# Kernel tuning notes

Measured on AMD Instinct MI355X. Metric: run time of the kernel, lower is better.

Reference implementation:

```python
import jax, jax.numpy as jnp
import numpy as np

N_NEURONS, D_MODEL, D_FF, N_PATTERNS, K_PATTERNS = 2048, 1024, 4096, 64, 4
B, S, K = 4, 2048, 8


def setup_inputs() -> dict:
    key = jax.random.key(0)
    ks = jax.random.split(key, 10)
    return {
        "x": jax.random.normal(ks[0], (B, S, D_MODEL), jnp.float32),
        "router_out": jax.random.normal(ks[1], (B, S, D_MODEL), jnp.float32),
        "topk_neuron_idx": jax.random.randint(ks[2], (B, S, K), 0, N_NEURONS),
        "topk_neuron_weights": jax.random.uniform(ks[3], (B, S, K), jnp.float32),
        "selected_neurons": jax.random.normal(ks[4], (B, S, K, D_MODEL), jnp.float32),
        "pattern_queries": jax.random.normal(ks[5], (N_PATTERNS, D_MODEL), jnp.float32) * 0.02,
        "gates": jax.random.normal(ks[6], (N_PATTERNS, D_FF), jnp.float32) * 0.02,
        "up_w": jax.random.normal(ks[7], (D_FF, D_MODEL), jnp.float32) / np.sqrt(D_MODEL),
        "up_b": jnp.zeros((D_FF,), jnp.float32),
        "down_w": jax.random.normal(ks[8], (D_MODEL, D_FF), jnp.float32) / np.sqrt(D_FF),
        "down_b": jnp.zeros((D_MODEL,), jnp.float32),
    }


def reference(x, router_out, topk_neuron_idx, topk_neuron_weights, selected_neurons,
              pattern_queries, gates, up_w, up_b, down_w, down_b):
    D = selected_neurons.shape[-1]
    # pattern scoring: [P, B, S, K]
    sim = jnp.einsum('pd,bskd->pbsk', pattern_queries, selected_neurons) / jnp.sqrt(jnp.float32(D))
    pattern_scores = jnp.einsum('pbsk,bsk->bsp', sim, topk_neuron_weights)  # weighted sum over K, permuted
    topk_scores, topk_pattern_idx = jax.lax.top_k(pattern_scores, K_PATTERNS)  # [B,S,k]
    topk_pattern_weights = jax.nn.softmax(topk_scores, axis=-1)
    selected_gates = gates[topk_pattern_idx]  # [B,S,k,d_ff]
    ffn_gate = jnp.einsum('bsk,bskf->bsf', topk_pattern_weights, selected_gates)
    h = jnp.einsum('bsd,fd->bsf', x, up_w) + up_b
    h = jax.nn.gelu(h * jax.nn.sigmoid(ffn_gate), approximate=False)
    return jnp.einsum('bsf,df->bsd', h, down_w) + down_b
```

## Files before the change

### kernel.cpp

```cpp
#include <hip/hip_runtime.h>
#include <hip/hip_bf16.h>
#include <math.h>

#define R_   8192
#define DM   1024
#define DFF  4096
#define NP   64
#define KN   8

typedef __bf16 bf16x8 __attribute__((ext_vector_type(8)));
typedef float  f32x4  __attribute__((ext_vector_type(4)));

__device__ __forceinline__ unsigned short f2bf(float f) {
  union { float f; unsigned u; } v; v.f = f;
  unsigned u = v.u;
  return (unsigned short)((u + 0x7FFFu + ((u >> 16) & 1u)) >> 16);
}

__device__ __forceinline__ float dot4(const float4 a, const float4 b) {
  return a.x * b.x + a.y * b.y + a.z * b.z + a.w * b.w;
}

__device__ __forceinline__ void fma4(float4& a, float w, const float4 s) {
  a.x += w * s.x; a.y += w * s.y; a.z += w * s.z; a.w += w * s.w;
}

__global__ __launch_bounds__(256) void cvt_bf16_kernel(
    const float* __restrict__ in, unsigned short* __restrict__ out, int n8) {
  int i = blockIdx.x * 256 + threadIdx.x;
  if (i >= n8) return;
  const float4* p = (const float4*)in + (size_t)i * 2;
  float4 a = p[0], b = p[1];
  uint4 r;
  r.x = (unsigned)f2bf(a.x) | ((unsigned)f2bf(a.y) << 16);
  r.y = (unsigned)f2bf(a.z) | ((unsigned)f2bf(a.w) << 16);
  r.z = (unsigned)f2bf(b.x) | ((unsigned)f2bf(b.y) << 16);
  r.w = (unsigned)f2bf(b.z) | ((unsigned)f2bf(b.w) << 16);
  ((uint4*)out)[i] = r;
}

__global__ __launch_bounds__(256) void vcomp_kernel(
    const float* __restrict__ sn,
    const float* __restrict__ tw,
    float* __restrict__ v)
{
  const int r = blockIdx.x;
  const int t = threadIdx.x;
  float w[KN];
#pragma unroll
  for (int k = 0; k < KN; ++k) w[k] = tw[(size_t)r * KN + k];
  const float* base = sn + (size_t)r * (KN * DM) + t * 4;
  float4 a = {0.f, 0.f, 0.f, 0.f};
#pragma unroll
  for (int k = 0; k < KN; ++k) fma4(a, w[k], *(const float4*)(base + k * DM));
  *(float4*)(v + (size_t)r * DM + t * 4) = a;
}

__global__ __launch_bounds__(256, 2) void score_kernel(
    const float* __restrict__ v,
    const float* __restrict__ pq,
    int*   __restrict__ out_idx,
    float* __restrict__ out_w)
{
  const int lane = threadIdx.x & 63;
  const int wave = threadIdx.x >> 6;
  const int pos0 = (blockIdx.x * 4 + wave) * 4;

  float4 vr[4][4];
#pragma unroll
  for (int p = 0; p < 4; ++p) {
    const float4* s = (const float4*)(v + (size_t)(pos0 + p) * DM + lane * 16);
    vr[p][0] = s[0]; vr[p][1] = s[1]; vr[p][2] = s[2]; vr[p][3] = s[3];
  }

  float sreg[4];
#pragma unroll 1
  for (int pat = 0; pat < NP; ++pat) {
    const float4* q = (const float4*)(pq + pat * DM + lane * 16);
    const float4 q0 = q[0], q1 = q[1], q2 = q[2], q3 = q[3];
    float part[4];
#pragma unroll
    for (int p = 0; p < 4; ++p)
      part[p] = dot4(q0, vr[p][0]) + dot4(q1, vr[p][1]) +
                dot4(q2, vr[p][2]) + dot4(q3, vr[p][3]);
#pragma unroll
    for (int off = 32; off >= 1; off >>= 1) {
#pragma unroll
      for (int p = 0; p < 4; ++p)
        part[p] += __shfl_xor(part[p], off, 64);
    }
    if (lane == pat) {
#pragma unroll
      for (int p = 0; p < 4; ++p) sreg[p] = part[p] * 0.03125f;
    }
  }

#pragma unroll
  for (int p = 0; p < 4; ++p) {
    float cur = sreg[p];
    float m0, m1, m2, m3; int i0, i1, i2, i3;
#define ARGMAX_STEP(MV, MI)                                   \
    {                                                         \
      float bv = cur; int bi = lane;                          \
      _Pragma("unroll")                                       \
      for (int off = 32; off >= 1; off >>= 1) {               \
        float ov = __shfl_xor(bv, off, 64);                   \
        int   oi = __shfl_xor(bi, off, 64);                   \
        if (ov > bv || (ov == bv && oi < bi)) { bv = ov; bi = oi; } \
      }                                                       \
      MV = bv; MI = bi;                                       \
      if (lane == bi) cur = -3.0e38f;                         \
    }
    ARGMAX_STEP(m0, i0) ARGMAX_STEP(m1, i1) ARGMAX_STEP(m2, i2) ARGMAX_STEP(m3, i3)
#undef ARGMAX_STEP
    const float e1 = __expf(m1 - m0), e2 = __expf(m2 - m0), e3 = __expf(m3 - m0);
    const float inv = 1.f / (1.f + e1 + e2 + e3);
    if (lane < 4) {
      const int r = pos0 + p;
      const int myi = (lane == 0) ? i0 : (lane == 1) ? i1 : (lane == 2) ? i2 : i3;
      const float mye = (lane == 0) ? 1.f : (lane == 1) ? e1 : (lane == 2) ? e2 : e3;
      out_idx[r * 4 + lane] = myi;
      out_w[r * 4 + lane] = mye * inv;
    }
  }
}

__device__ __forceinline__ void gll16(const void* g, void* l) {
  __builtin_amdgcn_global_load_lds(
      (const __attribute__((address_space(1))) unsigned int*)g,
      (__attribute__((address_space(3))) unsigned int*)l, 16, 0, 0);
}

template <int K, int N, int MODE>
__global__ __launch_bounds__(256, 2) void gemm_kernel(
    const unsigned short* __restrict__ A,
    const unsigned short* __restrict__ Bm,
    const float* __restrict__ bias,
    const int*   __restrict__ pidx,
    const float* __restrict__ pwt,
    const float* __restrict__ gates,
    void* __restrict__ Cout)
{
  __shared__ __align__(16) unsigned short As[128 * 32];
  __shared__ __align__(16) unsigned short Bs[128 * 32];
  const int tid  = threadIdx.x;
  const int lane = tid & 63;
  const int wid  = tid >> 6;
  const int wr   = wid >> 1;
  const int wc   = wid & 1;
  constexpr int NB = N / 128;
  const int brow = blockIdx.x / NB;
  const int bcol = blockIdx.x % NB;

  const unsigned short* Ab = A  + (size_t)brow * 128 * K;
  const unsigned short* Bb = Bm + (size_t)bcol * 128 * K;

  f32x4 acc[4][4];
#pragma unroll
  for (int m = 0; m < 4; ++m)
#pragma unroll
    for (int n = 0; n < 4; ++n)
      acc[m][n] = (f32x4){0.f, 0.f, 0.f, 0.f};

  const int srow = tid >> 2;
  const int scol = (tid & 3) * 8;
  char* ldsA = (char*)As + (tid >> 6) * 1024;
  char* ldsB = (char*)Bs + (tid >> 6) * 1024;

  const int arow = wr * 64 + (lane & 15);
  const int bro  = wc * 64 + (lane & 15);
  const int koff = (lane >> 4) * 8;

  for (int k0 = 0; k0 < K; k0 += 32) {
    if (k0) __syncthreads();
    gll16(Ab + (size_t)srow * K + k0 + scol,        ldsA);
    gll16(Ab + (size_t)(srow + 64) * K + k0 + scol, ldsA + 4096);
    gll16(Bb + (size_t)srow * K + k0 + scol,        ldsB);
    gll16(Bb + (size_t)(srow + 64) * K + k0 + scol, ldsB + 4096);
    __syncthreads();

    bf16x8 af[4], bfr[4];
#pragma unroll
    for (int m = 0; m < 4; ++m)
      af[m] = *(const bf16x8*)(As + (arow + m * 16) * 32 + koff);
#pragma unroll
    for (int n = 0; n < 4; ++n)
      bfr[n] = *(const bf16x8*)(Bs + (bro + n * 16) * 32 + koff);
#pragma unroll
    for (int m = 0; m < 4; ++m)
#pragma unroll
      for (int n = 0; n < 4; ++n)
        acc[m][n] = __builtin_amdgcn_mfma_f32_16x16x32_bf16(
            af[m], bfr[n], acc[m][n], 0, 0, 0);
  }

  const int crow0 = brow * 128 + wr * 64;
  const int ccol0 = bcol * 128 + wc * 64 + (lane & 15);
  const int rsub  = (lane >> 4) * 4;

  if (MODE == 0) {
    unsigned short* H = (unsigned short*)Cout;
#pragma unroll
    for (int m = 0; m < 4; ++m) {
      const int rbase = crow0 + m * 16 + rsub;
      int   ia[4][4];
      float wa[4][4];
#pragma unroll
      for (int j = 0; j < 4; ++j) {
        const int4   iq = *(const int4*)(pidx + (size_t)(rbase + j) * 4);
        const float4 wq = *(const float4*)(pwt + (size_t)(rbase + j) * 4);
        ia[j][0] = iq.x; ia[j][1] = iq.y; ia[j][2] = iq.z; ia[j][3] = iq.w;
        wa[j][0] = wq.x; wa[j][1] = wq.y; wa[j][2] = wq.z; wa[j][3] = wq.w;
      }
#pragma unroll
      for (int n = 0; n < 4; ++n) {
        const int col = ccol0 + n * 16;
        const float ub = bias[col];
#pragma unroll
        for (int j = 0; j < 4; ++j) {
          float g = wa[j][0] * gates[(size_t)ia[j][0] * DFF + col]
                  + wa[j][1] * gates[(size_t)ia[j][1] * DFF + col]
                  + wa[j][2] * gates[(size_t)ia[j][2] * DFF + col]
                  + wa[j][3] * gates[(size_t)ia[j][3] * DFF + col];
          const float u   = acc[m][n][j] + ub;
          const float val = u * (1.f / (1.f + __expf(-g)));
          const float h   = 0.5f * val * (1.f + erff(val * 0.70710678118654752f));
          H[(size_t)(rbase + j) * N + col] = f2bf(h);
        }
      }
    }
  } else {
    float* O = (float*)Cout;
#pragma unroll
    for (int m = 0; m < 4; ++m) {
      const int rbase = crow0 + m * 16 + rsub;
#pragma unroll
      for (int n = 0; n < 4; ++n) {
        const int col = ccol0 + n * 16;
        const float db = bias[col];
#pragma unroll
        for (int j = 0; j < 4; ++j)
          O[(size_t)(rbase + j) * N + col] = acc[m][n][j] + db;
      }
    }
  }
}

extern "C" void kernel_launch(void* const* d_in, const int* in_sizes, int n_in,
                              void* d_out, int out_size, void* d_ws, size_t ws_size,
                              hipStream_t stream) {
  const float* x     = (const float*)d_in[0];
  const float* tw    = (const float*)d_in[3];
  const float* sn    = (const float*)d_in[4];
  const float* pq    = (const float*)d_in[5];
  const float* gates = (const float*)d_in[6];
  const float* upw   = (const float*)d_in[7];
  const float* upb   = (const float*)d_in[8];
  const float* dnw   = (const float*)d_in[9];
  const float* dnb   = (const float*)d_in[10];
  float* out = (float*)d_out;

  char* p = (char*)d_ws;
  unsigned short* xb  = (unsigned short*)p; p += (size_t)R_ * DM * 2;
  unsigned short* uwb = (unsigned short*)p; p += (size_t)DFF * DM * 2;
  unsigned short* dwb = (unsigned short*)p; p += (size_t)DM * DFF * 2;
  unsigned short* H   = (unsigned short*)p; p += (size_t)R_ * DFF * 2;
  int*   pidx = (int*)p;   p += (size_t)R_ * 4 * sizeof(int);
  float* pwt  = (float*)p; p += (size_t)R_ * 4 * sizeof(float);
  float* vbuf = (float*)p; p += (size_t)R_ * DM * sizeof(float);

  cvt_bf16_kernel<<<(R_ * DM / 8) / 256, 256, 0, stream>>>(x, xb, R_ * DM / 8);
  cvt_bf16_kernel<<<(DFF * DM / 8) / 256, 256, 0, stream>>>(upw, uwb, DFF * DM / 8);
  cvt_bf16_kernel<<<(DM * DFF / 8) / 256, 256, 0, stream>>>(dnw, dwb, DM * DFF / 8);

  vcomp_kernel<<<R_, 256, 0, stream>>>(sn, tw, vbuf);
  score_kernel<<<R_ / 16, 256, 0, stream>>>(vbuf, pq, pidx, pwt);

  gemm_kernel<DM, DFF, 0><<<(R_ / 128) * (DFF / 128), 256, 0, stream>>>(
      xb, uwb, upb, pidx, pwt, gates, (void*)H);
  gemm_kernel<DFF, DM, 1><<<(R_ / 128) * (DM / 128), 256, 0, stream>>>(
      H, dwb, dnb, nullptr, nullptr, nullptr, (void*)out);
}
```

Before: 408.5 us.

## Replace LDS-staged GEMMs with direct-to-register double-buffered loads and larger tiles

Both GEMMs now load MFMA fragments straight from global memory into registers with a two-stage software double buffer, instead of staging tiles through LDS with two barriers per K step. Blocks grow to 512 threads with 256x256 (up-projection) and 256x128 (down-projection) tiles, a blockIdx swizzle improves L2 locality, and MFMA loops are bracketed with s_setprio. The aim is to remove LDS round trips and barrier stalls and to overlap loads with matrix math. In exchange, register pressure rises sharply (acc[8][4] plus two fragment sets), and without LDS sharing each wave reads its own operands from global memory, which raises cache traffic.

```diff
diff --git a/kernel.cpp b/kernel.cpp
--- a/kernel.cpp
+++ b/kernel.cpp
@@ -125,123 +125,155 @@
   }
 }
 
-__device__ __forceinline__ void gll16(const void* g, void* l) {
-  __builtin_amdgcn_global_load_lds(
-      (const __attribute__((address_space(1))) unsigned int*)g,
-      (__attribute__((address_space(3))) unsigned int*)l, 16, 0, 0);
-}
-
-template <int K, int N, int MODE>
-__global__ __launch_bounds__(256, 2) void gemm_kernel(
+
+#define MMLOOP(MF, ACCOFF, FA, FB)                                          \
+  __builtin_amdgcn_s_setprio(1);                                            \
+  _Pragma("unroll") for (int m_ = 0; m_ < MF; ++m_)                         \
+  _Pragma("unroll") for (int n_ = 0; n_ < 4; ++n_)                          \
+    acc[(ACCOFF) + m_][n_] = __builtin_amdgcn_mfma_f32_16x16x32_bf16(       \
+        FA[m_], FB[n_], acc[(ACCOFF) + m_][n_], 0, 0, 0);                   \
+  __builtin_amdgcn_s_setprio(0);
+
+__global__ __launch_bounds__(512, 2) void gemm1_kernel(
     const unsigned short* __restrict__ A,
     const unsigned short* __restrict__ Bm,
     const float* __restrict__ bias,
     const int*   __restrict__ pidx,
     const float* __restrict__ pwt,
     const float* __restrict__ gates,
-    void* __restrict__ Cout)
+    unsigned short* __restrict__ H)
 {
-  __shared__ __align__(16) unsigned short As[128 * 32];
-  __shared__ __align__(16) unsigned short Bs[128 * 32];
-  const int tid  = threadIdx.x;
-  const int lane = tid & 63;
-  const int wid  = tid >> 6;
-  const int wr   = wid >> 1;
-  const int wc   = wid & 1;
-  constexpr int NB = N / 128;
-  const int brow = blockIdx.x / NB;
-  const int bcol = blockIdx.x % NB;
-
-  const unsigned short* Ab = A  + (size_t)brow * 128 * K;
-  const unsigned short* Bb = Bm + (size_t)bcol * 128 * K;
+  constexpr int K_ = 1024, NT = 32;
+  const int lane = threadIdx.x & 63, wid = threadIdx.x >> 6;
+  const int wr = wid >> 2, wc = wid & 3;
+  const int cpx = gridDim.x >> 3;
+  const int swzb = ((int)blockIdx.x & 7) * cpx + ((int)blockIdx.x >> 3);
+  const int brow = swzb >> 4, bcol = swzb & 15;
+
+  const unsigned short* Ap =
+      A + (size_t)(brow * 256 + wr * 128 + (lane & 15)) * K_ + (lane >> 4) * 8;
+  const unsigned short* Bp =
+      Bm + (size_t)(bcol * 256 + wc * 64 + (lane & 15)) * K_ + (lane >> 4) * 8;
+
+  f32x4 acc[8][4];
+#pragma unroll
+  for (int m = 0; m < 8; ++m)
+#pragma unroll
+    for (int n = 0; n < 4; ++n) acc[m][n] = (f32x4){0.f, 0.f, 0.f, 0.f};
+
+  bf16x8 fa0[8], fb0[4], fa1[8], fb1[4];
+
+#define LD1(FA, FB, KT)                                                     \
+  { _Pragma("unroll") for (int m_ = 0; m_ < 8; ++m_)                        \
+      FA[m_] = *(const bf16x8*)(Ap + m_ * 16 * K_ + (KT) * 32);             \
+    _Pragma("unroll") for (int n_ = 0; n_ < 4; ++n_)                        \
+      FB[n_] = *(const bf16x8*)(Bp + n_ * 16 * K_ + (KT) * 32); }
+
+  LD1(fa0, fb0, 0)
+#pragma unroll 1
+  for (int kt = 0; kt < NT - 2; kt += 2) {
+    LD1(fa1, fb1, kt + 1)
+    MMLOOP(8, 0, fa0, fb0)
+    LD1(fa0, fb0, kt + 2)
+    MMLOOP(8, 0, fa1, fb1)
+  }
+  LD1(fa1, fb1, NT - 1)
+  MMLOOP(8, 0, fa0, fb0)
+  MMLOOP(8, 0, fa1, fb1)
+#undef LD1
+
+  const int crow0 = brow * 256 + wr * 128;
+  const int ccol0 = bcol * 256 + wc * 64 + (lane & 15);
+  const int rsub  = (lane >> 4) * 4;
+#pragma unroll
+  for (int m = 0; m < 8; ++m) {
+    const int rbase = crow0 + m * 16 + rsub;
+    int   ia[4][4];
+    float wa[4][4];
+#pragma unroll
+    for (int j = 0; j < 4; ++j) {
+      const int4   iq = *(const int4*)(pidx + (size_t)(rbase + j) * 4);
+      const float4 wq = *(const float4*)(pwt + (size_t)(rbase + j) * 4);
+      ia[j][0] = iq.x; ia[j][1] = iq.y; ia[j][2] = iq.z; ia[j][3] = iq.w;
+      wa[j][0] = wq.x; wa[j][1] = wq.y; wa[j][2] = wq.z; wa[j][3] = wq.w;
+    }
+#pragma unroll
+    for (int n = 0; n < 4; ++n) {
+      const int col = ccol0 + n * 16;
+      const float ub = bias[col];
+#pragma unroll
+      for (int j = 0; j < 4; ++j) {
+        float g = wa[j][0] * gates[(size_t)ia[j][0] * DFF + col]
+                + wa[j][1] * gates[(size_t)ia[j][1] * DFF + col]
+                + wa[j][2] * gates[(size_t)ia[j][2] * DFF + col]
+                + wa[j][3] * gates[(size_t)ia[j][3] * DFF + col];
+        const float u   = acc[m][n][j] + ub;
+        const float val = u * (1.f / (1.f + __expf(-g)));
+        const float h   = 0.5f * val * (1.f + erff(val * 0.70710678118654752f));
+        H[(size_t)(rbase + j) * DFF + col] = f2bf(h);
+      }
+    }
+  }
+}
+
+__global__ __launch_bounds__(512, 2) void gemm2_kernel(
+    const unsigned short* __restrict__ A,
+    const unsigned short* __restrict__ Bm,
+    const float* __restrict__ bias,
+    float* __restrict__ O)
+{
+  constexpr int K_ = 4096, NT = 128;
+  const int lane = threadIdx.x & 63, wid = threadIdx.x >> 6;
+  const int wr = wid >> 1, wc = wid & 1;
+  const int cpx = gridDim.x >> 3;
+  const int swzb = ((int)blockIdx.x & 7) * cpx + ((int)blockIdx.x >> 3);
+  const int brow = swzb >> 3, bcol = swzb & 7;
+
+  const unsigned short* Ap =
+      A + (size_t)(brow * 256 + wr * 64 + (lane & 15)) * K_ + (lane >> 4) * 8;
+  const unsigned short* Bp =
+      Bm + (size_t)(bcol * 128 + wc * 64 + (lane & 15)) * K_ + (lane >> 4) * 8;
 
   f32x4 acc[4][4];
 #pragma unroll
   for (int m = 0; m < 4; ++m)
 #pragma unroll
-    for (int n = 0; n < 4; ++n)
-      acc[m][n] = (f32x4){0.f, 0.f, 0.f, 0.f};
-
-  const int srow = tid >> 2;
-  const int scol = (tid & 3) * 8;
-  char* ldsA = (char*)As + (tid >> 6) * 1024;
-  char* ldsB = (char*)Bs + (tid >> 6) * 1024;
-
-  const int arow = wr * 64 + (lane & 15);
-  const int bro  = wc * 64 + (lane & 15);
-  const int koff = (lane >> 4) * 8;
-
-  for (int k0 = 0; k0 < K; k0 += 32) {
-    if (k0) __syncthreads();
-    gll16(Ab + (size_t)srow * K + k0 + scol,        ldsA);
-    gll16(Ab + (size_t)(srow + 64) * K + k0 + scol, ldsA + 4096);
-    gll16(Bb + (size_t)srow * K + k0 + scol,        ldsB);
-    gll16(Bb + (size_t)(srow + 64) * K + k0 + scol, ldsB + 4096);
-    __syncthreads();
-
-    bf16x8 af[4], bfr[4];
-#pragma unroll
-    for (int m = 0; m < 4; ++m)
-      af[m] = *(const bf16x8*)(As + (arow + m * 16) * 32 + koff);
-#pragma unroll
-    for (int n = 0; n < 4; ++n)
-      bfr[n] = *(const bf16x8*)(Bs + (bro + n * 16) * 32 + koff);
-#pragma unroll
-    for (int m = 0; m < 4; ++m)
-#pragma unroll
-      for (int n = 0; n < 4; ++n)
-        acc[m][n] = __builtin_amdgcn_mfma_f32_16x16x32_bf16(
-            af[m], bfr[n], acc[m][n], 0, 0, 0);
-  }
-
-  const int crow0 = brow * 128 + wr * 64;
+    for (int n = 0; n < 4; ++n) acc[m][n] = (f32x4){0.f, 0.f, 0.f, 0.f};
+
+  bf16x8 fa0[4], fb0[4], fa1[4], fb1[4];
+
+#define LD2(FA, FB, KT)                                                     \
+  { _Pragma("unroll") for (int m_ = 0; m_ < 4; ++m_)                        \
+      FA[m_] = *(const bf16x8*)(Ap + m_ * 16 * K_ + (KT) * 32);             \
+    _Pragma("unroll") for (int n_ = 0; n_ < 4; ++n_)                        \
+      FB[n_] = *(const bf16x8*)(Bp + n_ * 16 * K_ + (KT) * 32); }
+
+  LD2(fa0, fb0, 0)
+#pragma unroll 1
+  for (int kt = 0; kt < NT - 2; kt += 2) {
+    LD2(fa1, fb1, kt + 1)
+    MMLOOP(4, 0, fa0, fb0)
+    LD2(fa0, fb0, kt + 2)
+    MMLOOP(4, 0, fa1, fb1)
+  }
+  LD2(fa1, fb1, NT - 1)
+  MMLOOP(4, 0, fa0, fb0)
+  MMLOOP(4, 0, fa1, fb1)
+#undef LD2
+
+  const int crow0 = brow * 256 + wr * 64;
   const int ccol0 = bcol * 128 + wc * 64 + (lane & 15);
   const int rsub  = (lane >> 4) * 4;
-
-  if (MODE == 0) {
-    unsigned short* H = (unsigned short*)Cout;
-#pragma unroll
-    for (int m = 0; m < 4; ++m) {
-      const int rbase = crow0 + m * 16 + rsub;
-      int   ia[4][4];
-      float wa[4][4];
-#pragma unroll
-      for (int j = 0; j < 4; ++j) {
-        const int4   iq = *(const int4*)(pidx + (size_t)(rbase + j) * 4);
-        const float4 wq = *(const float4*)(pwt + (size_t)(rbase + j) * 4);
-        ia[j][0] = iq.x; ia[j][1] = iq.y; ia[j][2] = iq.z; ia[j][3] = iq.w;
-        wa[j][0] = wq.x; wa[j][1] = wq.y; wa[j][2] = wq.z; wa[j][3] = wq.w;
-      }
-#pragma unroll
-      for (int n = 0; n < 4; ++n) {
-        const int col = ccol0 + n * 16;
-        const float ub = bias[col];
-#pragma unroll
-        for (int j = 0; j < 4; ++j) {
-          float g = wa[j][0] * gates[(size_t)ia[j][0] * DFF + col]
-                  + wa[j][1] * gates[(size_t)ia[j][1] * DFF + col]
-                  + wa[j][2] * gates[(size_t)ia[j][2] * DFF + col]
-                  + wa[j][3] * gates[(size_t)ia[j][3] * DFF + col];
-          const float u   = acc[m][n][j] + ub;
-          const float val = u * (1.f / (1.f + __expf(-g)));
-          const float h   = 0.5f * val * (1.f + erff(val * 0.70710678118654752f));
-          H[(size_t)(rbase + j) * N + col] = f2bf(h);
-        }
-      }
-    }
-  } else {
-    float* O = (float*)Cout;
-#pragma unroll
-    for (int m = 0; m < 4; ++m) {
-      const int rbase = crow0 + m * 16 + rsub;
-#pragma unroll
-      for (int n = 0; n < 4; ++n) {
-        const int col = ccol0 + n * 16;
-        const float db = bias[col];
-#pragma unroll
-        for (int j = 0; j < 4; ++j)
-          O[(size_t)(rbase + j) * N + col] = acc[m][n][j] + db;
-      }
+#pragma unroll
+  for (int m = 0; m < 4; ++m) {
+    const int rbase = crow0 + m * 16 + rsub;
+#pragma unroll
+    for (int n = 0; n < 4; ++n) {
+      const int col = ccol0 + n * 16;
+      const float db = bias[col];
+#pragma unroll
+      for (int j = 0; j < 4; ++j)
+        O[(size_t)(rbase + j) * DM + col] = acc[m][n][j] + db;
     }
   }
 }
@@ -276,8 +308,8 @@
   vcomp_kernel<<<R_, 256, 0, stream>>>(sn, tw, vbuf);
   score_kernel<<<R_ / 16, 256, 0, stream>>>(vbuf, pq, pidx, pwt);
 
-  gemm_kernel<DM, DFF, 0><<<(R_ / 128) * (DFF / 128), 256, 0, stream>>>(
-      xb, uwb, upb, pidx, pwt, gates, (void*)H);
-  gemm_kernel<DFF, DM, 1><<<(R_ / 128) * (DM / 128), 256, 0, stream>>>(
-      H, dwb, dnb, nullptr, nullptr, nullptr, (void*)out);
-}
+  gemm1_kernel<<<(R_ / 256) * (DFF / 256), 512, 0, stream>>>(
+      xb, uwb, upb, pidx, pwt, gates, H);
+  gemm2_kernel<<<(R_ / 256) * (DM / 128), 512, 0, stream>>>(
+      H, dwb, dnb, out);
+}
```

Result: slower. 630.6 us (+54.4%).

## Rewrite GEMM with 256x128 tiles, triple-buffered LDS pipeline and swizzled layout

Applied to the files above, without the earlier changes.

Replaces the single-buffered 128x128 BK=32 GEMM with a 512-thread 256x128 tile kernel using BK=64, a three-stage global_load_lds pipeline with explicit vmcnt waits, XOR-swizzled LDS to avoid bank conflicts, and a block-index swizzle for L2 locality. It aims to hide global load latency and raise MFMA utilisation that the old load-sync-compute loop lacked. It uses 144KB of dynamic shared memory, which allows only one block per CU, and depends on hand-placed barriers and waitcnts being correct.

```diff
diff --git a/kernel.cpp b/kernel.cpp
--- a/kernel.cpp
+++ b/kernel.cpp
@@ -131,8 +131,10 @@
       (__attribute__((address_space(3))) unsigned int*)l, 16, 0, 0);
 }
 
-template <int K, int N, int MODE>
-__global__ __launch_bounds__(256, 2) void gemm_kernel(
+#define VMC(N) asm volatile("s_waitcnt vmcnt(%0)" ::"i"(N) : "memory")
+
+template <int K_, int NT, int NBN, int MODE>
+__global__ __launch_bounds__(512) void gemm_kernel(
     const unsigned short* __restrict__ A,
     const unsigned short* __restrict__ Bm,
     const float* __restrict__ bias,
@@ -141,60 +143,87 @@
     const float* __restrict__ gates,
     void* __restrict__ Cout)
 {
-  __shared__ __align__(16) unsigned short As[128 * 32];
-  __shared__ __align__(16) unsigned short Bs[128 * 32];
-  const int tid  = threadIdx.x;
-  const int lane = tid & 63;
-  const int wid  = tid >> 6;
-  const int wr   = wid >> 1;
-  const int wc   = wid & 1;
-  constexpr int NB = N / 128;
-  const int brow = blockIdx.x / NB;
-  const int bcol = blockIdx.x % NB;
-
-  const unsigned short* Ab = A  + (size_t)brow * 128 * K;
-  const unsigned short* Bb = Bm + (size_t)bcol * 128 * K;
+  extern __shared__ char smem[];
+  const int tid = threadIdx.x, lane = tid & 63, wid = tid >> 6;
+  const int wr = wid >> 1, wc = wid & 1;
+
+  const int cpx = gridDim.x >> 3;
+  const int swzb = ((int)blockIdx.x & 7) * cpx + ((int)blockIdx.x >> 3);
+  int brow, bcol;
+  if (MODE == 0) { brow = swzb / NBN; bcol = swzb % NBN; }
+  else           { bcol = swzb >> 5;  brow = swzb & 31;  }
+
+  const unsigned short* Ab = A  + (size_t)brow * 256 * K_;
+  const unsigned short* Bb = Bm + (size_t)bcol * 128 * K_;
+
+  const size_t aoff = (size_t)(wid * 8 + (lane >> 3)) * K_ +
+                      ((lane & 7) ^ (lane >> 3)) * 8;
+  const int sw0 = (((lane >> 4))     ^ (lane & 7)) * 16;
+  const int sw1 = ((4 + (lane >> 4)) ^ (lane & 7)) * 16;
+  const int aRdB = wr * 8192 + (lane & 15) * 128;
+  const int bRdB = 32768 + wc * 8192 + (lane & 15) * 128;
 
   f32x4 acc[4][4];
 #pragma unroll
   for (int m = 0; m < 4; ++m)
 #pragma unroll
-    for (int n = 0; n < 4; ++n)
-      acc[m][n] = (f32x4){0.f, 0.f, 0.f, 0.f};
-
-  const int srow = tid >> 2;
-  const int scol = (tid & 3) * 8;
-  char* ldsA = (char*)As + (tid >> 6) * 1024;
-  char* ldsB = (char*)Bs + (tid >> 6) * 1024;
-
-  const int arow = wr * 64 + (lane & 15);
-  const int bro  = wc * 64 + (lane & 15);
-  const int koff = (lane >> 4) * 8;
-
-  for (int k0 = 0; k0 < K; k0 += 32) {
-    if (k0) __syncthreads();
-    gll16(Ab + (size_t)srow * K + k0 + scol,        ldsA);
-    gll16(Ab + (size_t)(srow + 64) * K + k0 + scol, ldsA + 4096);
-    gll16(Bb + (size_t)srow * K + k0 + scol,        ldsB);
-    gll16(Bb + (size_t)(srow + 64) * K + k0 + scol, ldsB + 4096);
-    __syncthreads();
-
-    bf16x8 af[4], bfr[4];
-#pragma unroll
-    for (int m = 0; m < 4; ++m)
-      af[m] = *(const bf16x8*)(As + (arow + m * 16) * 32 + koff);
-#pragma unroll
-    for (int n = 0; n < 4; ++n)
-      bfr[n] = *(const bf16x8*)(Bs + (bro + n * 16) * 32 + koff);
-#pragma unroll
-    for (int m = 0; m < 4; ++m)
-#pragma unroll
-      for (int n = 0; n < 4; ++n)
-        acc[m][n] = __builtin_amdgcn_mfma_f32_16x16x32_bf16(
-            af[m], bfr[n], acc[m][n], 0, 0, 0);
-  }
-
-  const int crow0 = brow * 128 + wr * 64;
+    for (int n = 0; n < 4; ++n) acc[m][n] = (f32x4){0.f, 0.f, 0.f, 0.f};
+
+#define STG(OS, KT) {                                                         \
+    _Pragma("unroll") for (int h_ = 0; h_ < 4; ++h_)                          \
+      gll16(Ab + (KT) * 64 + (size_t)h_ * 64 * K_ + aoff,                     \
+            smem + (OS) + h_ * 8192 + wid * 1024);                            \
+    _Pragma("unroll") for (int h_ = 0; h_ < 2; ++h_)                          \
+      gll16(Bb + (KT) * 64 + (size_t)h_ * 64 * K_ + aoff,                     \
+            smem + (OS) + 32768 + h_ * 8192 + wid * 1024); }
+
+#define RDS(OB, SW)                                                           \
+    { const char* pa = smem + (OB) + aRdB;                                    \
+      const char* pb = smem + (OB) + bRdB;                                    \
+      _Pragma("unroll") for (int m_ = 0; m_ < 4; ++m_)                        \
+        a[m_] = *(const bf16x8*)(pa + m_ * 2048 + (SW));                      \
+      _Pragma("unroll") for (int n_ = 0; n_ < 4; ++n_)                        \
+        b[n_] = *(const bf16x8*)(pb + n_ * 2048 + (SW)); }
+
+#define MIDSYNC                                                               \
+    __builtin_amdgcn_s_barrier();                                             \
+    asm volatile("s_waitcnt lgkmcnt(0)" ::: "memory");                        \
+    __builtin_amdgcn_sched_barrier(0);
+
+#define MF16                                                                  \
+    __builtin_amdgcn_s_setprio(1);                                            \
+    _Pragma("unroll") for (int m_ = 0; m_ < 4; ++m_)                          \
+    _Pragma("unroll") for (int n_ = 0; n_ < 4; ++n_)                          \
+      acc[m_][n_] = __builtin_amdgcn_mfma_f32_16x16x32_bf16(                  \
+          a[m_], b[n_], acc[m_][n_], 0, 0, 0);                                \
+    __builtin_amdgcn_s_setprio(0);                                            \
+    __builtin_amdgcn_s_barrier();
+
+  STG(0, 0)
+  STG(49152, 1)
+  VMC(6);
+  __builtin_amdgcn_s_barrier();
+
+  int o0 = 0, o1 = 49152, o2 = 98304;
+#pragma unroll 1
+  for (int t = 0; t < NT; ++t) {
+    bf16x8 a[4], b[4];
+    RDS(o0, sw0)
+    if (t + 2 < NT) STG(o2, t + 2)
+    MIDSYNC
+    MF16
+    RDS(o0, sw1)
+    if (t < NT - 2) { VMC(6); } else { VMC(0); }
+    MIDSYNC
+    MF16
+    const int tmp = o0; o0 = o1; o1 = o2; o2 = tmp;
+  }
+#undef STG
+#undef RDS
+#undef MIDSYNC
+#undef MF16
+
+  const int crow0 = brow * 256 + wr * 64;
   const int ccol0 = bcol * 128 + wc * 64 + (lane & 15);
   const int rsub  = (lane >> 4) * 4;
 
@@ -225,7 +254,7 @@
           const float u   = acc[m][n][j] + ub;
           const float val = u * (1.f / (1.f + __expf(-g)));
           const float h   = 0.5f * val * (1.f + erff(val * 0.70710678118654752f));
-          H[(size_t)(rbase + j) * N + col] = f2bf(h);
+          H[(size_t)(rbase + j) * DFF + col] = f2bf(h);
         }
       }
     }
@@ -240,7 +269,7 @@
         const float db = bias[col];
 #pragma unroll
         for (int j = 0; j < 4; ++j)
-          O[(size_t)(rbase + j) * N + col] = acc[m][n][j] + db;
+          O[(size_t)(rbase + j) * DM + col] = acc[m][n][j] + db;
       }
     }
   }
@@ -276,8 +305,15 @@
   vcomp_kernel<<<R_, 256, 0, stream>>>(sn, tw, vbuf);
   score_kernel<<<R_ / 16, 256, 0, stream>>>(vbuf, pq, pidx, pwt);
 
-  gemm_kernel<DM, DFF, 0><<<(R_ / 128) * (DFF / 128), 256, 0, stream>>>(
+  auto* k1 = gemm_kernel<DM, 16, 32, 0>;
+  auto* k2 = gemm_kernel<DFF, 64, 8, 1>;
+  hipFuncSetAttribute((const void*)k1,
+                      hipFuncAttributeMaxDynamicSharedMemorySize, 147456);
+  hipFuncSetAttribute((const void*)k2,
+                      hipFuncAttributeMaxDynamicSharedMemorySize, 147456);
+
+  k1<<<(R_ / 256) * (DFF / 128), 512, 147456, stream>>>(
       xb, uwb, upb, pidx, pwt, gates, (void*)H);
-  gemm_kernel<DFF, DM, 1><<<(R_ / 128) * (DM / 128), 256, 0, stream>>>(
+  k2<<<(R_ / 256) * (DM / 128), 512, 147456, stream>>>(
       H, dwb, dnb, nullptr, nullptr, nullptr, (void*)out);
 }
```

After: 380.1 us. 1.07x faster.

## Switch GEMMs to 32x32x16 MFMA with swizzled LDS and larger up-proj tiles

Applied to the files above, without the earlier changes.

Splits the templated GEMM into two specialised kernels that use 32x32x16 bf16 MFMA instead of 16x16x32. The up-projection tile grows to 256x128, block indices are remapped to group work across XCDs, and an XOR swizzle is applied to LDS loads and reads to avoid bank conflicts. The goal is fewer LDS reads per MFMA, better operand reuse and better L2 locality. The tradeoffs are more accumulator registers and more LDS in gemm1, which may reduce occupancy, and the gate epilogue still gathers from global memory per element.

```diff
diff --git a/kernel.cpp b/kernel.cpp
--- a/kernel.cpp
+++ b/kernel.cpp
@@ -10,6 +10,7 @@
 
 typedef __bf16 bf16x8 __attribute__((ext_vector_type(8)));
 typedef float  f32x4  __attribute__((ext_vector_type(4)));
+typedef float  f32x16 __attribute__((ext_vector_type(16)));
 
 __device__ __forceinline__ unsigned short f2bf(float f) {
   union { float f; unsigned u; } v; v.f = f;
@@ -131,117 +132,180 @@
       (__attribute__((address_space(3))) unsigned int*)l, 16, 0, 0);
 }
 
-template <int K, int N, int MODE>
-__global__ __launch_bounds__(256, 2) void gemm_kernel(
+
+__global__ __launch_bounds__(256, 2) void gemm1_kernel(
     const unsigned short* __restrict__ A,
     const unsigned short* __restrict__ Bm,
     const float* __restrict__ bias,
     const int*   __restrict__ pidx,
     const float* __restrict__ pwt,
     const float* __restrict__ gates,
-    void* __restrict__ Cout)
+    unsigned short* __restrict__ H)
 {
-  __shared__ __align__(16) unsigned short As[128 * 32];
-  __shared__ __align__(16) unsigned short Bs[128 * 32];
-  const int tid  = threadIdx.x;
-  const int lane = tid & 63;
-  const int wid  = tid >> 6;
-  const int wr   = wid >> 1;
-  const int wc   = wid & 1;
-  constexpr int NB = N / 128;
-  const int brow = blockIdx.x / NB;
-  const int bcol = blockIdx.x % NB;
-
-  const unsigned short* Ab = A  + (size_t)brow * 128 * K;
-  const unsigned short* Bb = Bm + (size_t)bcol * 128 * K;
-
-  f32x4 acc[4][4];
+  constexpr int K_ = 1024;
+  __shared__ __align__(16) char smem[24576];
+  const int tid = threadIdx.x, lane = tid & 63, wid = tid >> 6;
+  const int wr = wid >> 1, wc = wid & 1;
+
+  const int cpx = gridDim.x >> 3;
+  const int swzb = ((int)blockIdx.x & 7) * cpx + ((int)blockIdx.x >> 3);
+  const int brow = swzb & 31, bcol = swzb >> 5;
+
+  const unsigned short* Ab = A  + (size_t)brow * 256 * K_;
+  const unsigned short* Bb = Bm + (size_t)bcol * 128 * K_;
+
+  const int slotg = ((tid & 3) ^ ((tid >> 3) & 3)) * 8;
+  const int srow  = tid >> 2;
+  const int rA    = (lane & 31) * 64;
+  const int swk0  = (((lane >> 5))     ^ ((lane >> 1) & 3)) * 16;
+  const int swk1  = ((2 + (lane >> 5)) ^ ((lane >> 1) & 3)) * 16;
+
+  f32x16 acc[4][2];
 #pragma unroll
   for (int m = 0; m < 4; ++m)
 #pragma unroll
-    for (int n = 0; n < 4; ++n)
-      acc[m][n] = (f32x4){0.f, 0.f, 0.f, 0.f};
-
-  const int srow = tid >> 2;
-  const int scol = (tid & 3) * 8;
-  char* ldsA = (char*)As + (tid >> 6) * 1024;
-  char* ldsB = (char*)Bs + (tid >> 6) * 1024;
-
-  const int arow = wr * 64 + (lane & 15);
-  const int bro  = wc * 64 + (lane & 15);
-  const int koff = (lane >> 4) * 8;
-
-  for (int k0 = 0; k0 < K; k0 += 32) {
+    for (int n = 0; n < 2; ++n)
+#pragma unroll
+      for (int e = 0; e < 16; ++e) acc[m][n][e] = 0.f;
+
+#pragma unroll 1
+  for (int k0 = 0; k0 < K_; k0 += 32) {
     if (k0) __syncthreads();
-    gll16(Ab + (size_t)srow * K + k0 + scol,        ldsA);
-    gll16(Ab + (size_t)(srow + 64) * K + k0 + scol, ldsA + 4096);
-    gll16(Bb + (size_t)srow * K + k0 + scol,        ldsB);
-    gll16(Bb + (size_t)(srow + 64) * K + k0 + scol, ldsB + 4096);
+#pragma unroll
+    for (int c = 0; c < 4; ++c)
+      gll16(Ab + (size_t)(c * 64 + srow) * K_ + k0 + slotg,
+            smem + c * 4096 + wid * 1024);
+#pragma unroll
+    for (int c = 0; c < 2; ++c)
+      gll16(Bb + (size_t)(c * 64 + srow) * K_ + k0 + slotg,
+            smem + 16384 + c * 4096 + wid * 1024);
     __syncthreads();
 
-    bf16x8 af[4], bfr[4];
-#pragma unroll
-    for (int m = 0; m < 4; ++m)
-      af[m] = *(const bf16x8*)(As + (arow + m * 16) * 32 + koff);
-#pragma unroll
-    for (int n = 0; n < 4; ++n)
-      bfr[n] = *(const bf16x8*)(Bs + (bro + n * 16) * 32 + koff);
-#pragma unroll
-    for (int m = 0; m < 4; ++m)
-#pragma unroll
-      for (int n = 0; n < 4; ++n)
-        acc[m][n] = __builtin_amdgcn_mfma_f32_16x16x32_bf16(
-            af[m], bfr[n], acc[m][n], 0, 0, 0);
+#pragma unroll
+    for (int ks = 0; ks < 2; ++ks) {
+      const int sw = ks ? swk1 : swk0;
+      const char* pa = smem + wr * 8192 + rA + sw;
+      const char* pb = smem + 16384 + wc * 4096 + rA + sw;
+      bf16x8 af[4], bf[2];
+#pragma unroll
+      for (int m = 0; m < 4; ++m) af[m] = *(const bf16x8*)(pa + m * 2048);
+#pragma unroll
+      for (int n = 0; n < 2; ++n) bf[n] = *(const bf16x8*)(pb + n * 2048);
+#pragma unroll
+      for (int m = 0; m < 4; ++m)
+#pragma unroll
+        for (int n = 0; n < 2; ++n)
+          acc[m][n] = __builtin_amdgcn_mfma_f32_32x32x16_bf16(
+              af[m], bf[n], acc[m][n], 0, 0, 0);
+    }
+  }
+
+  const int crow0 = brow * 256 + wr * 128;
+  const int ccol0 = bcol * 128 + wc * 64 + (lane & 31);
+  const int rhalf = (lane >> 5) * 4;
+  const float ub0 = bias[ccol0];
+  const float ub1 = bias[ccol0 + 32];
+#pragma unroll
+  for (int m = 0; m < 4; ++m) {
+#pragma unroll
+    for (int reg = 0; reg < 16; ++reg) {
+      const int row = crow0 + m * 32 + (reg & 3) + 8 * (reg >> 2) + rhalf;
+      const int4   iq = *(const int4*)(pidx + (size_t)row * 4);
+      const float4 wq = *(const float4*)(pwt + (size_t)row * 4);
+      const float* g0 = gates + (size_t)iq.x * DFF;
+      const float* g1 = gates + (size_t)iq.y * DFF;
+      const float* g2 = gates + (size_t)iq.z * DFF;
+      const float* g3 = gates + (size_t)iq.w * DFF;
+#pragma unroll
+      for (int n = 0; n < 2; ++n) {
+        const int col = ccol0 + n * 32;
+        const float g = wq.x * g0[col] + wq.y * g1[col] +
+                        wq.z * g2[col] + wq.w * g3[col];
+        const float u   = acc[m][n][reg] + (n ? ub1 : ub0);
+        const float val = u * (1.f / (1.f + __expf(-g)));
+        const float h   = 0.5f * val * (1.f + erff(val * 0.70710678118654752f));
+        H[(size_t)row * DFF + col] = f2bf(h);
+      }
+    }
+  }
+}
+
+__global__ __launch_bounds__(256, 2) void gemm2_kernel(
+    const unsigned short* __restrict__ A,
+    const unsigned short* __restrict__ Bm,
+    const float* __restrict__ bias,
+    float* __restrict__ O)
+{
+  constexpr int K_ = 4096;
+  __shared__ __align__(16) char smem[16384];
+  const int tid = threadIdx.x, lane = tid & 63, wid = tid >> 6;
+  const int wr = wid >> 1, wc = wid & 1;
+
+  const int cpx = gridDim.x >> 3;
+  const int swzb = ((int)blockIdx.x & 7) * cpx + ((int)blockIdx.x >> 3);
+  const int brow = swzb & 63, bcol = swzb >> 6;
+
+  const unsigned short* Ab = A  + (size_t)brow * 128 * K_;
+  const unsigned short* Bb = Bm + (size_t)bcol * 128 * K_;
+
+  const int slotg = ((tid & 3) ^ ((tid >> 3) & 3)) * 8;
+  const int srow  = tid >> 2;
+  const int rA    = (lane & 31) * 64;
+  const int swk0  = (((lane >> 5))     ^ ((lane >> 1) & 3)) * 16;
+  const int swk1  = ((2 + (lane >> 5)) ^ ((lane >> 1) & 3)) * 16;
+
+  f32x16 acc[2][2];
+#pragma unroll
+  for (int m = 0; m < 2; ++m)
+#pragma unroll
+    for (int n = 0; n < 2; ++n)
+#pragma unroll
+      for (int e = 0; e < 16; ++e) acc[m][n][e] = 0.f;
+
+#pragma unroll 1
+  for (int k0 = 0; k0 < K_; k0 += 32) {
+    if (k0) __syncthreads();
+#pragma unroll
+    for (int c = 0; c < 2; ++c)
+      gll16(Ab + (size_t)(c * 64 + srow) * K_ + k0 + slotg,
+            smem + c * 4096 + wid * 1024);
+#pragma unroll
+    for (int c = 0; c < 2; ++c)
+      gll16(Bb + (size_t)(c * 64 + srow) * K_ + k0 + slotg,
+            smem + 8192 + c * 4096 + wid * 1024);
+    __syncthreads();
+
+#pragma unroll
+    for (int ks = 0; ks < 2; ++ks) {
+      const int sw = ks ? swk1 : swk0;
+      const char* pa = smem + wr * 4096 + rA + sw;
+      const char* pb = smem + 8192 + wc * 4096 + rA + sw;
+      bf16x8 af[2], bf[2];
+#pragma unroll
+      for (int m = 0; m < 2; ++m) af[m] = *(const bf16x8*)(pa + m * 2048);
+#pragma unroll
+      for (int n = 0; n < 2; ++n) bf[n] = *(const bf16x8*)(pb + n * 2048);
+#pragma unroll
+      for (int m = 0; m < 2; ++m)
+#pragma unroll
+        for (int n = 0; n < 2; ++n)
+          acc[m][n] = __builtin_amdgcn_mfma_f32_32x32x16_bf16(
+              af[m], bf[n], acc[m][n], 0, 0, 0);
+    }
   }
 
   const int crow0 = brow * 128 + wr * 64;
-  const int ccol0 = bcol * 128 + wc * 64 + (lane & 15);
-  const int rsub  = (lane >> 4) * 4;
-
-  if (MODE == 0) {
-    unsigned short* H = (unsigned short*)Cout;
-#pragma unroll
-    for (int m = 0; m < 4; ++m) {
-      const int rbase = crow0 + m * 16 + rsub;
-      int   ia[4][4];
-      float wa[4][4];
-#pragma unroll
-      for (int j = 0; j < 4; ++j) {
-        const int4   iq = *(const int4*)(pidx + (size_t)(rbase + j) * 4);
-        const float4 wq = *(const float4*)(pwt + (size_t)(rbase + j) * 4);
-        ia[j][0] = iq.x; ia[j][1] = iq.y; ia[j][2] = iq.z; ia[j][3] = iq.w;
-        wa[j][0] = wq.x; wa[j][1] = wq.y; wa[j][2] = wq.z; wa[j][3] = wq.w;
-      }
-#pragma unroll
-      for (int n = 0; n < 4; ++n) {
-        const int col = ccol0 + n * 16;
-        const float ub = bias[col];
-#pragma unroll
-        for (int j = 0; j < 4; ++j) {
-          float g = wa[j][0] * gates[(size_t)ia[j][0] * DFF + col]
-                  + wa[j][1] * gates[(size_t)ia[j][1] * DFF + col]
-                  + wa[j][2] * gates[(size_t)ia[j][2] * DFF + col]
-                  + wa[j][3] * gates[(size_t)ia[j][3] * DFF + col];
-          const float u   = acc[m][n][j] + ub;
-          const float val = u * (1.f / (1.f + __expf(-g)));
-          const float h   = 0.5f * val * (1.f + erff(val * 0.70710678118654752f));
-          H[(size_t)(rbase + j) * N + col] = f2bf(h);
-        }
-      }
-    }
-  } else {
-    float* O = (float*)Cout;
-#pragma unroll
-    for (int m = 0; m < 4; ++m) {
-      const int rbase = crow0 + m * 16 + rsub;
-#pragma unroll
-      for (int n = 0; n < 4; ++n) {
-        const int col = ccol0 + n * 16;
-        const float db = bias[col];
-#pragma unroll
-        for (int j = 0; j < 4; ++j)
-          O[(size_t)(rbase + j) * N + col] = acc[m][n][j] + db;
-      }
+  const int ccol0 = bcol * 128 + wc * 64 + (lane & 31);
+  const int rhalf = (lane >> 5) * 4;
+  const float db0 = bias[ccol0];
+  const float db1 = bias[ccol0 + 32];
+#pragma unroll
+  for (int m = 0; m < 2; ++m) {
+#pragma unroll
+    for (int reg = 0; reg < 16; ++reg) {
+      const int row = crow0 + m * 32 + (reg & 3) + 8 * (reg >> 2) + rhalf;
+      O[(size_t)row * DM + ccol0]      = acc[m][0][reg] + db0;
+      O[(size_t)row * DM + ccol0 + 32] = acc[m][1][reg] + db1;
     }
   }
 }
@@ -276,8 +340,8 @@
   vcomp_kernel<<<R_, 256, 0, stream>>>(sn, tw, vbuf);
   score_kernel<<<R_ / 16, 256, 0, stream>>>(vbuf, pq, pidx, pwt);
 
-  gemm_kernel<DM, DFF, 0><<<(R_ / 128) * (DFF / 128), 256, 0, stream>>>(
-      xb, uwb, upb, pidx, pwt, gates, (void*)H);
-  gemm_kernel<DFF, DM, 1><<<(R_ / 128) * (DM / 128), 256, 0, stream>>>(
-      H, dwb, dnb, nullptr, nullptr, nullptr, (void*)out);
-}
+  gemm1_kernel<<<(R_ / 256) * (DFF / 128), 256, 0, stream>>>(
+      xb, uwb, upb, pidx, pwt, gates, H);
+  gemm2_kernel<<<(R_ / 128) * (DM / 128), 256, 0, stream>>>(
+      H, dwb, dnb, out);
+}
```

Measured after the change: 447.1 us. +9.5%, slower.
